# Performance work log

Measured on AMD Instinct MI355X. Metric: run time of the kernel, lower is better.

The kernel has to match this reference:

```python
import jax, jax.numpy as jnp
import numpy as np

H = 128      # mamba_num_heads
P = 64       # mamba_head_dim
G = 8        # n_groups
N = 128      # ssm_state_size
CS = 128     # chunk_size
K = 4        # conv kernel size
DIM = 4096
INTER = H * P                 # 8192
CONV_DIM = INTER + 2 * G * N  # 10240
EPS = 1e-5


def segment_sum(x):
    # x: (..., T). Returns (..., T, T) with [i,j] = sum_{k=j+1..i} x[k] for i>=j, else -inf.
    T = x.shape[-1]
    x = jnp.repeat(x[..., None], T, axis=-1)
    x = jnp.where(jnp.tril(jnp.ones((T, T), dtype=bool), -1), x, 0.0)
    s = jnp.cumsum(x, axis=-2)
    return jnp.where(jnp.tril(jnp.ones((T, T), dtype=bool), 0), s, -jnp.inf)


def setup_inputs() -> dict:
    key = jax.random.key(0)
    ks = jax.random.split(key, 8)
    Bz, L = 1, 2048
    return {
        "hidden_states": jax.random.normal(ks[0], (Bz, L, DIM), jnp.float32),
        "in_proj_w": jax.random.normal(ks[1], (INTER + CONV_DIM + H, DIM), jnp.float32) * 0.02,
        "conv_w": jax.random.normal(ks[2], (CONV_DIM, 1, K), jnp.float32) * 0.2,
        "conv_b": jnp.zeros((CONV_DIM,), jnp.float32),
        "dt_bias": jnp.log(jnp.exp(jnp.linspace(0.001, 0.1, H)) - 1.0).astype(jnp.float32),
        "A_log": jnp.log(jax.random.uniform(ks[3], (H,), jnp.float32, 1.0, 16.0)),
        "D": jnp.ones((H,), jnp.float32),
        "norm_w": jnp.ones((INTER,), jnp.float32),
        "out_proj_w": jax.random.normal(ks[4], (DIM, INTER), jnp.float32) * 0.02,
    }


def reference(hidden_states, in_proj_w, conv_w, conv_b, dt_bias, A_log, D, norm_w, out_proj_w):
    Bz, L, _ = hidden_states.shape
    proj = hidden_states @ in_proj_w.T  # (B,L,INTER+CONV_DIM+H)
    gate = proj[..., :INTER]
    hBC = proj[..., INTER:INTER + CONV_DIM]
    dt = proj[..., INTER + CONV_DIM:]

    # causal depthwise conv1d + silu
    xc = jnp.transpose(hBC, (0, 2, 1))  # (B, CONV_DIM, L)
    xc = jax.lax.conv_general_dilated(
        xc, conv_w, (1,), [(K - 1, 0)],
        dimension_numbers=("NCH", "OIH", "NCH"),
        feature_group_count=CONV_DIM) + conv_b[None, :, None]
    hBC = jax.nn.silu(jnp.transpose(xc, (0, 2, 1)))

    x = hBC[..., :INTER].reshape(Bz, L, H, P)
    Bm = hBC[..., INTER:INTER + G * N].reshape(Bz, L, G, N)
    Cm = hBC[..., INTER + G * N:].reshape(Bz, L, G, N)
    Bm = jnp.repeat(Bm, H // G, axis=2)  # (B,L,H,N)
    Cm = jnp.repeat(Cm, H // G, axis=2)

    dt = jax.nn.softplus(dt + dt_bias)  # (B,L,H); dt_limit=(0,inf) -> no clamp
    A = -jnp.exp(A_log)                 # (H,)

    D_residual = D[None, None, :, None] * x
    A_dt = A[None, None, :] * dt        # (B,L,H)
    x_dt = x * dt[..., None]

    Cn = L // CS  # L chosen divisible by chunk_size (pad_size = 0)
    Ac = jnp.transpose(A_dt.reshape(Bz, Cn, CS, H), (0, 3, 1, 2))  # (B,H,Cn,CS)
    xch = x_dt.reshape(Bz, Cn, CS, H, P)
    Bch = Bm.reshape(Bz, Cn, CS, H, N)
    Cch = Cm.reshape(Bz, Cn, CS, H, N)

    A_cumsum = jnp.cumsum(Ac, axis=-1)
    Lmat = jnp.exp(segment_sum(Ac))  # (B,H,Cn,CS,CS)

    # 1. intra-chunk diagonal block outputs
    Gm = jnp.einsum("bclhn,bcshn->bclsh", Cch, Bch)
    M = Gm * jnp.transpose(Lmat, (0, 2, 3, 4, 1))
    Y_diag = jnp.einsum("bclsh,bcshp->bclhp", M, xch)

    # 2. per-chunk end states
    decay_states = jnp.exp(A_cumsum[..., -1:] - A_cumsum)  # (B,H,Cn,CS)
    B_decay = Bch * jnp.transpose(decay_states, (0, 2, 3, 1))[..., None]
    states = jnp.einsum("bclhn,bclhp->bchpn", B_decay, xch)

    # 3. inter-chunk recurrence via segment_sum over chunk decays
    states_cat = jnp.concatenate([jnp.zeros_like(states[:, :1]), states], axis=1)  # (B,Cn+1,H,P,N)
    A_last = jnp.pad(A_cumsum[..., -1], ((0, 0), (0, 0), (1, 0)))
    decay_chunk = jnp.exp(segment_sum(A_last))  # (B,H,Cn+1,Cn+1)
    new_states = jnp.einsum("bhij,bjhpn->bihpn", decay_chunk, states_cat)
    states = new_states[:, :-1]  # (B,Cn,H,P,N)

    # 4. state -> output conversion
    state_decay = jnp.transpose(jnp.exp(A_cumsum), (0, 2, 3, 1))  # (B,Cn,CS,H)
    Y_off = jnp.einsum("bclhn,bchpn->bclhp", Cch, states) * state_decay[..., None]

    y = (Y_diag + Y_off).reshape(Bz, L, H, P) + D_residual
    y = y.reshape(Bz, L, INTER)

    # gated RMSNorm (computed in fp32)
    var = jnp.mean(jnp.square(y), axis=-1, keepdims=True)
    y = y * jax.lax.rsqrt(var + EPS) * norm_w
    y = y * jax.nn.silu(gate)

    return y @ out_proj_w.T
```

## Files before the change

kernel.cpp:

```cpp
#include <hip/hip_runtime.h>
#include <hip/hip_bf16.h>

#define L_    2048
#define DIM_  4096
#define H_    128
#define P_    64
#define G_    8
#define NST_  128
#define CS_   128
#define NC_   16
#define INTER_ 8192
#define CONVD_ 10240
#define NPROJ_ 18560

typedef unsigned short u16;
typedef __attribute__((ext_vector_type(8))) __bf16 bf16x8;
typedef __attribute__((ext_vector_type(4))) float f32x4;

__device__ __forceinline__ u16 f2bf(float f) {
  unsigned u = __float_as_uint(f);
  u += 0x7FFFu + ((u >> 16) & 1u);
  return (u16)(u >> 16);
}
__device__ __forceinline__ float bf2f(u16 v) {
  return __uint_as_float(((unsigned)v) << 16);
}
__device__ __forceinline__ float silu_f(float x) {
  return x / (1.f + expf(-x));
}

__device__ __forceinline__ f32x4 mfma_bf16(bf16x8 a, bf16x8 b, f32x4 c) {
  return __builtin_amdgcn_mfma_f32_16x16x32_bf16(a, b, c, 0, 0, 0);
}

__device__ __forceinline__ void glds16(const u16* g, u16* l) {
  const auto* gp = (const __attribute__((address_space(1))) unsigned int*)(unsigned long long)(g);
  auto* lp = (__attribute__((address_space(3))) unsigned int*)(unsigned long long)(l);
  __builtin_amdgcn_global_load_lds(gp, lp, 16, 0, 0);
}

#define S_BARRIER() asm volatile("s_barrier" ::: "memory")

__global__ __launch_bounds__(256) void cast_k(const float* __restrict__ src,
                                              u16* __restrict__ dst, int n4) {
  int i = blockIdx.x * 256 + threadIdx.x;
  if (i >= n4) return;
  float4 v = ((const float4*)src)[i];
  ushort4 o = make_ushort4(f2bf(v.x), f2bf(v.y), f2bf(v.z), f2bf(v.w));
  ((ushort4*)dst)[i] = o;
}

template <int MI, int SWZ>
__global__ __launch_bounds__(512) void gemm_p(const u16* __restrict__ A,
                                              const u16* __restrict__ B,
                                              float* __restrict__ C,
                                              int M, int N, int K, int nbm) {
  constexpr int BM = MI * 32;
  constexpr int ATILE2 = BM * 32;
  constexpr int BTILE2 = 256 * 32;
  constexpr int TILE2 = ATILE2 + BTILE2;
  constexpr int AJ = BM / 128;
  __shared__ __align__(16) u16 lds[4 * TILE2];

  const int tid = threadIdx.x;
  const int lane = tid & 63, wv = tid >> 6;
  const int wvm = wv >> 2, wvn = wv & 3;
  const int lr = lane & 15, kg = lane >> 4;
  const int cofs = ((kg * 16) ^ ((lr << 3) & 0x30)) >> 1;

  int lin = blockIdx.x;
  if (SWZ) { const int ch = gridDim.x >> 3; lin = (lin & 7) * ch + (lin >> 3); }
  const int bm = (lin % nbm) * BM;
  const int bn = (lin / nbm) * 256;

  const u16* gA[2];
  const u16* gB[2];
  int dA[2], dB[2];
#pragma unroll
  for (int j = 0; j < AJ; ++j) {
    int o = (j * 512 + tid) * 16;
    int b = o ^ ((o >> 3) & 0x30);
    gA[j] = A + (size_t)(bm + (b >> 6)) * K + ((b & 63) >> 1);
    dA[j] = o >> 1;
  }
#pragma unroll
  for (int j = 0; j < 2; ++j) {
    int o = (j * 512 + tid) * 16;
    int b = o ^ ((o >> 3) & 0x30);
    gB[j] = B + (size_t)(bn + (b >> 6)) * K + ((b & 63) >> 1);
    dB[j] = ATILE2 + (o >> 1);
  }

  const int NT = K >> 5;
  f32x4 acc[MI][4] = {};

#pragma unroll
  for (int tt = 0; tt < 3; ++tt) {
#pragma unroll
    for (int j = 0; j < AJ; ++j) glds16(gA[j] + tt * 32, &lds[tt * TILE2 + dA[j]]);
#pragma unroll
    for (int j = 0; j < 2; ++j)  glds16(gB[j] + tt * 32, &lds[tt * TILE2 + dB[j]]);
  }
  if constexpr (AJ == 2) { asm volatile("s_waitcnt vmcnt(8)" ::: "memory"); }
  else                   { asm volatile("s_waitcnt vmcnt(6)" ::: "memory"); }
  S_BARRIER();

  for (int t = 0; t < NT; ++t) {
    const int rb = (t & 3) * TILE2;
    const int sb = ((t + 3) & 3) * TILE2;
    const bool st = (t + 3 < NT);
    const int abase = rb + (wvm * (MI * 16) + lr) * 32 + cofs;
    const int bbase = rb + ATILE2 + (wvn * 64 + lr) * 32 + cofs;

    bf16x8 av[4], bv[4];
#pragma unroll
    for (int mi = 0; mi < 4; ++mi) av[mi] = *(const bf16x8*)&lds[abase + mi * 512];
#pragma unroll
    for (int ni = 0; ni < 4; ++ni) bv[ni] = *(const bf16x8*)&lds[bbase + ni * 512];

    if constexpr (MI == 8) {
      if (st) {
#pragma unroll
        for (int j = 0; j < 2; ++j) glds16(gA[j] + (t + 3) * 32, &lds[sb + dA[j]]);
      }
      S_BARRIER();
      __builtin_amdgcn_s_setprio(1);
#pragma unroll
      for (int mi = 0; mi < 4; ++mi)
#pragma unroll
        for (int ni = 0; ni < 4; ++ni)
          acc[mi][ni] = mfma_bf16(av[mi], bv[ni], acc[mi][ni]);
      __builtin_amdgcn_s_setprio(0);
      S_BARRIER();
      bf16x8 aw[4];
#pragma unroll
      for (int mi = 0; mi < 4; ++mi) aw[mi] = *(const bf16x8*)&lds[abase + (mi + 4) * 512];
      if (st) {
#pragma unroll
        for (int j = 0; j < 2; ++j) glds16(gB[j] + (t + 3) * 32, &lds[sb + dB[j]]);
      }
      S_BARRIER();
      __builtin_amdgcn_s_setprio(1);
#pragma unroll
      for (int mi = 0; mi < 4; ++mi)
#pragma unroll
        for (int ni = 0; ni < 4; ++ni)
          acc[mi + 4][ni] = mfma_bf16(aw[mi], bv[ni], acc[mi + 4][ni]);
      __builtin_amdgcn_s_setprio(0);
      if (st)              { asm volatile("s_waitcnt vmcnt(8)" ::: "memory"); }
      else if (t + 2 < NT) { asm volatile("s_waitcnt vmcnt(4)" ::: "memory"); }
      else if (t + 1 < NT) { asm volatile("s_waitcnt vmcnt(0)" ::: "memory"); }
      S_BARRIER();
    } else {
      if (st) {
        glds16(gA[0] + (t + 3) * 32, &lds[sb + dA[0]]);
#pragma unroll
        for (int j = 0; j < 2; ++j) glds16(gB[j] + (t + 3) * 32, &lds[sb + dB[j]]);
      }
      S_BARRIER();
      __builtin_amdgcn_s_setprio(1);
#pragma unroll
      for (int mi = 0; mi < 4; ++mi)
#pragma unroll
        for (int ni = 0; ni < 4; ++ni)
          acc[mi][ni] = mfma_bf16(av[mi], bv[ni], acc[mi][ni]);
      __builtin_amdgcn_s_setprio(0);
      if (st)              { asm volatile("s_waitcnt vmcnt(6)" ::: "memory"); }
      else if (t + 2 < NT) { asm volatile("s_waitcnt vmcnt(3)" ::: "memory"); }
      else if (t + 1 < NT) { asm volatile("s_waitcnt vmcnt(0)" ::: "memory"); }
      S_BARRIER();
    }
  }

#pragma unroll
  for (int mi = 0; mi < MI; ++mi)
#pragma unroll
    for (int ni = 0; ni < 4; ++ni) {
      f32x4 a4 = acc[mi][ni];
#pragma unroll
      for (int r = 0; r < 4; ++r) {
        int row = bm + wvm * (MI * 16) + mi * 16 + kg * 4 + r;
        int col = bn + wvn * 64 + ni * 16 + lr;
        if (col < N) C[(size_t)row * N + col] = a4[r];
      }
    }
}

__global__ __launch_bounds__(256) void conv_silu(const float* __restrict__ proj,
                                                 const float* __restrict__ cw,
                                                 const float* __restrict__ cb,
                                                 u16* __restrict__ xo,
                                                 u16* __restrict__ Bo,
                                                 u16* __restrict__ Co) {
  int ci = blockIdx.x * 256 + threadIdx.x;
  int l = blockIdx.y;
  const float* w = cw + ci * 4;
  float a = cb[ci];
#pragma unroll
  for (int k = 0; k < 4; ++k) {
    int ls = l - 3 + k;
    if (ls >= 0) a += proj[(size_t)ls * NPROJ_ + INTER_ + ci] * w[k];
  }
  u16 bv = f2bf(silu_f(a));
  if (ci < INTER_)             xo[(size_t)l * INTER_ + ci] = bv;
  else if (ci < INTER_ + 1024) Bo[(size_t)l * 1024 + (ci - INTER_)] = bv;
  else                         Co[(size_t)l * 1024 + (ci - INTER_ - 1024)] = bv;
}

__global__ __launch_bounds__(256) void dt_k(const float* __restrict__ proj,
                                            const float* __restrict__ dt_bias,
                                            float* __restrict__ dtb) {
  int i = blockIdx.x * 256 + threadIdx.x;
  int l = i >> 7, h = i & 127;
  float z = proj[(size_t)l * NPROJ_ + (INTER_ + CONVD_) + h] + dt_bias[h];
  dtb[i] = (z > 20.f) ? z : log1pf(expf(z));
}

__global__ __launch_bounds__(256) void ssm_intra(const u16* __restrict__ xb,
                                                 const u16* __restrict__ Bb,
                                                 const u16* __restrict__ Cb,
                                                 const float* __restrict__ dtb,
                                                 const float* __restrict__ A_log,
                                                 const float* __restrict__ Dp,
                                                 float* __restrict__ acum_g,
                                                 float* __restrict__ states,
                                                 float* __restrict__ Y) {
  __shared__ __align__(16) u16 bufM[128 * 136];
  __shared__ __align__(16) u16 buf3[64 * 136];
  __shared__ float s_dt[128];
  __shared__ float s_ac[128];
  const int c = blockIdx.x, h = blockIdx.y, g = h >> 4;
  const int tid = threadIdx.x;
  const int lane = tid & 63, wv = tid >> 6;
  const int lr = lane & 15, kg = lane >> 4;

  float Ah = -expf(A_log[h]);
  if (tid < 128) {
    float dv = dtb[(size_t)(c * 128 + tid) * 128 + h];
    s_dt[tid] = dv;
    s_ac[tid] = Ah * dv;
  }
  __syncthreads();
  for (int off = 1; off < 128; off <<= 1) {
    float v = 0.f;
    if (tid < 128 && tid >= off) v = s_ac[tid - off];
    __syncthreads();
    if (tid < 128) s_ac[tid] += v;
    __syncthreads();
  }
  if (tid < 128) acum_g[((size_t)c * 128 + h) * 128 + tid] = s_ac[tid];

  for (int it = 0; it < 32; ++it) {
    int idx = tid + 256 * it;
    int p = idx & 63, srow = idx >> 6;
    float xv = bf2f(xb[(size_t)(c * 128 + srow) * INTER_ + h * 64 + p]);
    buf3[p * 136 + srow] = f2bf(xv * s_dt[srow]);
  }

  const u16* Cbase = Cb + (size_t)c * 128 * 1024 + g * 128;
  const u16* Bbase = Bb + (size_t)c * 128 * 1024 + g * 128;
  const int wm = (wv >> 1) << 6, wn = (wv & 1) << 6;
  f32x4 S[4][4] = {};
  for (int ks = 0; ks < 128; ks += 32) {
    bf16x8 av[4], bv[4];
#pragma unroll
    for (int mi = 0; mi < 4; ++mi)
      av[mi] = *(const bf16x8*)(Cbase + (size_t)(wm + mi * 16 + lr) * 1024 + ks + kg * 8);
#pragma unroll
    for (int ni = 0; ni < 4; ++ni)
      bv[ni] = *(const bf16x8*)(Bbase + (size_t)(wn + ni * 16 + lr) * 1024 + ks + kg * 8);
#pragma unroll
    for (int mi = 0; mi < 4; ++mi)
#pragma unroll
      for (int ni = 0; ni < 4; ++ni)
        S[mi][ni] = mfma_bf16(av[mi], bv[ni], S[mi][ni]);
  }

#pragma unroll
  for (int mi = 0; mi < 4; ++mi)
#pragma unroll
    for (int ni = 0; ni < 4; ++ni) {
      f32x4 sv = S[mi][ni];
#pragma unroll
      for (int r = 0; r < 4; ++r) {
        int l = wm + mi * 16 + kg * 4 + r;
        int s = wn + ni * 16 + lr;
        float mv = 0.f;
        if (l >= s) mv = sv[r] * expf(s_ac[l] - s_ac[s]);
        bufM[l * 136 + s] = f2bf(mv);
      }
    }
  __syncthreads();

  f32x4 yacc[2][4] = {};
  for (int ks = 0; ks < 128; ks += 32) {
    bf16x8 am[2], bx[4];
#pragma unroll
    for (int mi = 0; mi < 2; ++mi)
      am[mi] = *(const bf16x8*)&bufM[(32 * wv + mi * 16 + lr) * 136 + ks + kg * 8];
#pragma unroll
    for (int ni = 0; ni < 4; ++ni)
      bx[ni] = *(const bf16x8*)&buf3[(ni * 16 + lr) * 136 + ks + kg * 8];
#pragma unroll
    for (int mi = 0; mi < 2; ++mi)
#pragma unroll
      for (int ni = 0; ni < 4; ++ni)
        yacc[mi][ni] = mfma_bf16(am[mi], bx[ni], yacc[mi][ni]);
  }
  float Dh = Dp[h];
#pragma unroll
  for (int mi = 0; mi < 2; ++mi)
#pragma unroll
    for (int ni = 0; ni < 4; ++ni) {
      f32x4 yv = yacc[mi][ni];
#pragma unroll
      for (int r = 0; r < 4; ++r) {
        int l = 32 * wv + mi * 16 + kg * 4 + r;
        int p = ni * 16 + lr;
        size_t o = (size_t)(c * 128 + l) * INTER_ + h * 64 + p;
        Y[o] = yv[r] + Dh * bf2f(xb[o]);
      }
    }

  float aclast = s_ac[127];
  __syncthreads();
  for (int it = 0; it < 64; ++it) {
    int idx = tid + 256 * it;
    int n = idx & 127, lrow = idx >> 7;
    float bvv = bf2f(Bb[(size_t)(c * 128 + lrow) * 1024 + g * 128 + n]);
    bufM[n * 136 + lrow] = f2bf(bvv * expf(aclast - s_ac[lrow]));
  }
  __syncthreads();
  f32x4 st[8] = {};
  for (int ks = 0; ks < 128; ks += 32) {
    bf16x8 ax = *(const bf16x8*)&buf3[(16 * wv + lr) * 136 + ks + kg * 8];
#pragma unroll
    for (int ni = 0; ni < 8; ++ni) {
      bf16x8 bn = *(const bf16x8*)&bufM[(ni * 16 + lr) * 136 + ks + kg * 8];
      st[ni] = mfma_bf16(ax, bn, st[ni]);
    }
  }
#pragma unroll
  for (int ni = 0; ni < 8; ++ni) {
    f32x4 sv = st[ni];
#pragma unroll
    for (int r = 0; r < 4; ++r) {
      int p = 16 * wv + kg * 4 + r;
      int n = ni * 16 + lr;
      states[(((size_t)c * 128 + h) * 64 + p) * 128 + n] = sv[r];
    }
  }
}

__global__ __launch_bounds__(256) void scan_k(float* __restrict__ states,
                                              const float* __restrict__ acum_g) {
  int j = blockIdx.x * 256 + threadIdx.x;
  int h = j >> 13;
  float run = 0.f;
  float* p = states + j;
  for (int c = 0; c < NC_; ++c) {
    float dk = expf(acum_g[((size_t)c * 128 + h) * 128 + 127]);
    float v = p[(size_t)c * 1048576];
    p[(size_t)c * 1048576] = run;
    run = run * dk + v;
  }
}

__global__ __launch_bounds__(256) void ssm_off(const u16* __restrict__ Cb,
                                               const float* __restrict__ states,
                                               const float* __restrict__ acum_g,
                                               float* __restrict__ Y) {
  const int c = blockIdx.x, h = blockIdx.y, g = h >> 4;
  const int tid = threadIdx.x, lane = tid & 63, wv = tid >> 6;
  const int lr = lane & 15, kg = lane >> 4;
  const u16* Cbase = Cb + (size_t)c * 128 * 1024 + g * 128;
  const float* sbase = states + ((size_t)c * 128 + h) * 64 * 128;
  f32x4 acc[2][4] = {};
  for (int ks = 0; ks < 128; ks += 32) {
    bf16x8 av[2], bv[4];
#pragma unroll
    for (int mi = 0; mi < 2; ++mi)
      av[mi] = *(const bf16x8*)(Cbase + (size_t)(32 * wv + mi * 16 + lr) * 1024 + ks + kg * 8);
#pragma unroll
    for (int ni = 0; ni < 4; ++ni) {
      const float* sp = sbase + (size_t)(ni * 16 + lr) * 128 + ks + kg * 8;
      float4 u0 = *(const float4*)sp;
      float4 u1 = *(const float4*)(sp + 4);
      union { bf16x8 v; u16 u[8]; } t;
      t.u[0] = f2bf(u0.x); t.u[1] = f2bf(u0.y); t.u[2] = f2bf(u0.z); t.u[3] = f2bf(u0.w);
      t.u[4] = f2bf(u1.x); t.u[5] = f2bf(u1.y); t.u[6] = f2bf(u1.z); t.u[7] = f2bf(u1.w);
      bv[ni] = t.v;
    }
#pragma unroll
    for (int mi = 0; mi < 2; ++mi)
#pragma unroll
      for (int ni = 0; ni < 4; ++ni)
        acc[mi][ni] = mfma_bf16(av[mi], bv[ni], acc[mi][ni]);
  }
  const float* ac = acum_g + ((size_t)c * 128 + h) * 128;
#pragma unroll
  for (int mi = 0; mi < 2; ++mi)
#pragma unroll
    for (int ni = 0; ni < 4; ++ni) {
      f32x4 a4 = acc[mi][ni];
#pragma unroll
      for (int r = 0; r < 4; ++r) {
        int l = 32 * wv + mi * 16 + kg * 4 + r;
        int p = ni * 16 + lr;
        size_t o = (size_t)(c * 128 + l) * INTER_ + h * 64 + p;
        Y[o] += expf(ac[l]) * a4[r];
      }
    }
}

__global__ __launch_bounds__(256) void norm_gate(const float* __restrict__ Y,
                                                 const float* __restrict__ proj,
                                                 const float* __restrict__ norm_w,
                                                 u16* __restrict__ ybf) {
  const int l = blockIdx.x, tid = threadIdx.x;
  const float* yr = Y + (size_t)l * INTER_;
  float ss = 0.f;
  for (int i = tid; i < 2048; i += 256) {
    float4 v = ((const float4*)yr)[i];
    ss += v.x * v.x + v.y * v.y + v.z * v.z + v.w * v.w;
  }
  for (int off = 32; off > 0; off >>= 1) ss += __shfl_down(ss, off, 64);
  __shared__ float red[4];
  if ((tid & 63) == 0) red[tid >> 6] = ss;
  __syncthreads();
  float rs = rsqrtf((red[0] + red[1] + red[2] + red[3]) * (1.f / 8192.f) + 1e-5f);
  const float* gr = proj + (size_t)l * NPROJ_;
  for (int i = tid; i < 2048; i += 256) {
    float4 v = ((const float4*)yr)[i];
    float4 gv = ((const float4*)gr)[i];
    float4 nw = ((const float4*)norm_w)[i];
    ushort4 o = make_ushort4(f2bf(v.x * rs * nw.x * silu_f(gv.x)),
                             f2bf(v.y * rs * nw.y * silu_f(gv.y)),
                             f2bf(v.z * rs * nw.z * silu_f(gv.z)),
                             f2bf(v.w * rs * nw.w * silu_f(gv.w)));
    ((ushort4*)ybf)[(size_t)l * 2048 + i] = o;
  }
}

extern "C" void kernel_launch(void* const* d_in, const int* in_sizes, int n_in,
                              void* d_out, int out_size, void* d_ws, size_t ws_size,
                              hipStream_t stream) {
  const float* hs      = (const float*)d_in[0];
  const float* w_in    = (const float*)d_in[1];
  const float* conv_w  = (const float*)d_in[2];
  const float* conv_b  = (const float*)d_in[3];
  const float* dt_bias = (const float*)d_in[4];
  const float* A_log   = (const float*)d_in[5];
  const float* Dv      = (const float*)d_in[6];
  const float* norm_w  = (const float*)d_in[7];
  const float* w_out   = (const float*)d_in[8];
  float* out = (float*)d_out;

  char* ws = (char*)d_ws;
  u16*   hs_bf   = (u16*)(ws + 0);
  u16*   win_bf  = (u16*)(ws + 16777216);
  float* states  = (float*)(ws + 16777216);
  float* Yb      = (float*)(ws + 16777216 + 67108864);
  float* proj    = (float*)(ws + 168820736);
  u16*   wout_bf = (u16*)(ws + 168820736);
  u16*   xb      = (u16*)(ws + 320864256);
  u16*   ybf     = (u16*)(ws + 320864256);
  u16*   Bb      = (u16*)(ws + 354418688);
  u16*   Cbuf    = (u16*)(ws + 358612992);
  float* dtb     = (float*)(ws + 362807296);
  float* acum    = (float*)(ws + 363855872);

  cast_k<<<(L_ * DIM_ / 4 + 255) / 256, 256, 0, stream>>>(hs, hs_bf, L_ * DIM_ / 4);
  cast_k<<<(NPROJ_ * DIM_ / 4 + 255) / 256, 256, 0, stream>>>(w_in, win_bf, NPROJ_ * DIM_ / 4);
  gemm_p<8, 1><<<dim3(8 * 73), 512, 0, stream>>>(hs_bf, win_bf, proj, L_, NPROJ_, DIM_, 8);
  conv_silu<<<dim3(CONVD_ / 256, L_), 256, 0, stream>>>(proj, conv_w, conv_b, xb, Bb, Cbuf);
  dt_k<<<(L_ * H_) / 256, 256, 0, stream>>>(proj, dt_bias, dtb);
  ssm_intra<<<dim3(NC_, H_), 256, 0, stream>>>(xb, Bb, Cbuf, dtb, A_log, Dv, acum, states, Yb);
  scan_k<<<(H_ * P_ * NST_) / 256, 256, 0, stream>>>(states, acum);
  ssm_off<<<dim3(NC_, H_), 256, 0, stream>>>(Cbuf, states, acum, Yb);
  norm_gate<<<L_, 256, 0, stream>>>(Yb, proj, norm_w, ybf);
  cast_k<<<(DIM_ * INTER_ / 4 + 255) / 256, 256, 0, stream>>>(w_out, wout_bf, DIM_ * INTER_ / 4);
  gemm_p<4, 0><<<dim3(16 * 16), 512, 0, stream>>>(ybf, wout_bf, out, L_, DIM_, INTER_, 16);
}
```

Before: 1.390 ms.

## Double-buffer GEMM LDS fragments in registers to overlap reads with MFMA

Rewrites the main loop of the bf16 GEMM so that the LDS fragments for the next k-tile are loaded into a second register set while MFMAs run on the current one, ping-ponging between two register buffers. The loop is unrolled by two and uses one barrier per tile instead of two or three, with the MI==8 and MI==4 paths unified. The goal is to hide LDS read latency and cut barrier stalls. In exchange it raises register pressure (two full fragment sets plus accumulators), which may lower occupancy or cause spills. It also assumes NT is even.

```diff
diff --git a/kernel.cpp b/kernel.cpp
--- a/kernel.cpp
+++ b/kernel.cpp
@@ -60,6 +60,8 @@
   constexpr int BTILE2 = 256 * 32;
   constexpr int TILE2 = ATILE2 + BTILE2;
   constexpr int AJ = BM / 128;
+  constexpr int LC = AJ + 2;
+  constexpr int NF = MI + 4;
   __shared__ __align__(16) u16 lds[4 * TILE2];
 
   const int tid = threadIdx.x;
@@ -101,76 +103,54 @@
 #pragma unroll
     for (int j = 0; j < 2; ++j)  glds16(gB[j] + tt * 32, &lds[tt * TILE2 + dB[j]]);
   }
-  if constexpr (AJ == 2) { asm volatile("s_waitcnt vmcnt(8)" ::: "memory"); }
-  else                   { asm volatile("s_waitcnt vmcnt(6)" ::: "memory"); }
+  asm volatile("s_waitcnt vmcnt(%0)" :: "n"(2 * LC) : "memory");
   S_BARRIER();
 
-  for (int t = 0; t < NT; ++t) {
-    const int rb = (t & 3) * TILE2;
-    const int sb = ((t + 3) & 3) * TILE2;
-    const bool st = (t + 3 < NT);
-    const int abase = rb + (wvm * (MI * 16) + lr) * 32 + cofs;
-    const int bbase = rb + ATILE2 + (wvn * 64 + lr) * 32 + cofs;
-
-    bf16x8 av[4], bv[4];
-#pragma unroll
-    for (int mi = 0; mi < 4; ++mi) av[mi] = *(const bf16x8*)&lds[abase + mi * 512];
-#pragma unroll
-    for (int ni = 0; ni < 4; ++ni) bv[ni] = *(const bf16x8*)&lds[bbase + ni * 512];
-
-    if constexpr (MI == 8) {
-      if (st) {
-#pragma unroll
-        for (int j = 0; j < 2; ++j) glds16(gA[j] + (t + 3) * 32, &lds[sb + dA[j]]);
-      }
-      S_BARRIER();
-      __builtin_amdgcn_s_setprio(1);
-#pragma unroll
-      for (int mi = 0; mi < 4; ++mi)
-#pragma unroll
-        for (int ni = 0; ni < 4; ++ni)
-          acc[mi][ni] = mfma_bf16(av[mi], bv[ni], acc[mi][ni]);
-      __builtin_amdgcn_s_setprio(0);
-      S_BARRIER();
-      bf16x8 aw[4];
-#pragma unroll
-      for (int mi = 0; mi < 4; ++mi) aw[mi] = *(const bf16x8*)&lds[abase + (mi + 4) * 512];
-      if (st) {
-#pragma unroll
-        for (int j = 0; j < 2; ++j) glds16(gB[j] + (t + 3) * 32, &lds[sb + dB[j]]);
-      }
-      S_BARRIER();
-      __builtin_amdgcn_s_setprio(1);
-#pragma unroll
-      for (int mi = 0; mi < 4; ++mi)
-#pragma unroll
-        for (int ni = 0; ni < 4; ++ni)
-          acc[mi + 4][ni] = mfma_bf16(aw[mi], bv[ni], acc[mi + 4][ni]);
-      __builtin_amdgcn_s_setprio(0);
-      if (st)              { asm volatile("s_waitcnt vmcnt(8)" ::: "memory"); }
-      else if (t + 2 < NT) { asm volatile("s_waitcnt vmcnt(4)" ::: "memory"); }
-      else if (t + 1 < NT) { asm volatile("s_waitcnt vmcnt(0)" ::: "memory"); }
-      S_BARRIER();
-    } else {
-      if (st) {
-        glds16(gA[0] + (t + 3) * 32, &lds[sb + dA[0]]);
-#pragma unroll
-        for (int j = 0; j < 2; ++j) glds16(gB[j] + (t + 3) * 32, &lds[sb + dB[j]]);
-      }
-      S_BARRIER();
-      __builtin_amdgcn_s_setprio(1);
-#pragma unroll
-      for (int mi = 0; mi < 4; ++mi)
-#pragma unroll
-        for (int ni = 0; ni < 4; ++ni)
-          acc[mi][ni] = mfma_bf16(av[mi], bv[ni], acc[mi][ni]);
-      __builtin_amdgcn_s_setprio(0);
-      if (st)              { asm volatile("s_waitcnt vmcnt(6)" ::: "memory"); }
-      else if (t + 2 < NT) { asm volatile("s_waitcnt vmcnt(3)" ::: "memory"); }
-      else if (t + 1 < NT) { asm volatile("s_waitcnt vmcnt(0)" ::: "memory"); }
-      S_BARRIER();
-    }
-  }
+  bf16x8 Ra[NF], Rb[NF];
+#pragma unroll
+  for (int mi = 0; mi < MI; ++mi)
+    Ra[mi] = *(const bf16x8*)&lds[(wvm * (MI * 16) + mi * 16 + lr) * 32 + cofs];
+#pragma unroll
+  for (int ni = 0; ni < 4; ++ni)
+    Ra[MI + ni] = *(const bf16x8*)&lds[ATILE2 + (wvn * 64 + ni * 16 + lr) * 32 + cofs];
+
+#define TILE_BODY(T, CUR, NXT)                                                          \
+  do {                                                                                  \
+    const int t_ = (T);                                                                 \
+    if (t_ + 3 < NT) {                                                                  \
+      const int sb_ = ((t_ + 3) & 3) * TILE2;                                           \
+      _Pragma("unroll") for (int j = 0; j < AJ; ++j)                                    \
+        glds16(gA[j] + (t_ + 3) * 32, &lds[sb_ + dA[j]]);                               \
+      _Pragma("unroll") for (int j = 0; j < 2; ++j)                                     \
+        glds16(gB[j] + (t_ + 3) * 32, &lds[sb_ + dB[j]]);                               \
+    }                                                                                   \
+    if (t_ + 1 < NT) {                                                                  \
+      if (t_ + 3 < NT)      asm volatile("s_waitcnt vmcnt(%0)" :: "n"(2 * LC) : "memory"); \
+      else if (t_ + 2 < NT) asm volatile("s_waitcnt vmcnt(%0)" :: "n"(LC) : "memory");  \
+      else                  asm volatile("s_waitcnt vmcnt(0)" ::: "memory");            \
+    }                                                                                   \
+    asm volatile("s_waitcnt lgkmcnt(0)" ::: "memory");                                  \
+    S_BARRIER();                                                                        \
+    if (t_ + 1 < NT) {                                                                  \
+      const int nb_ = ((t_ + 1) & 3) * TILE2;                                           \
+      _Pragma("unroll") for (int mi = 0; mi < MI; ++mi)                                 \
+        NXT[mi] = *(const bf16x8*)&lds[nb_ + (wvm * (MI * 16) + mi * 16 + lr) * 32 + cofs]; \
+      _Pragma("unroll") for (int ni = 0; ni < 4; ++ni)                                  \
+        NXT[MI + ni] = *(const bf16x8*)&lds[nb_ + ATILE2 + (wvn * 64 + ni * 16 + lr) * 32 + cofs]; \
+    }                                                                                   \
+    __builtin_amdgcn_sched_barrier(0);                                                  \
+    __builtin_amdgcn_s_setprio(1);                                                      \
+    _Pragma("unroll") for (int mi = 0; mi < MI; ++mi)                                   \
+      _Pragma("unroll") for (int ni = 0; ni < 4; ++ni)                                  \
+        acc[mi][ni] = mfma_bf16(CUR[mi], CUR[MI + ni], acc[mi][ni]);                    \
+    __builtin_amdgcn_s_setprio(0);                                                      \
+  } while (0)
+
+  for (int t = 0; t < NT; t += 2) {
+    TILE_BODY(t, Ra, Rb);
+    TILE_BODY(t + 1, Rb, Ra);
+  }
+#undef TILE_BODY
 
 #pragma unroll
   for (int mi = 0; mi < MI; ++mi)
```

Result: no change. 1.400 ms (+0.7%).
